# Kernel optimization log

Measured on AMD Instinct MI355X. Metric: run time of the kernel, lower is better.

## Reference

```python
import jax, jax.numpy as jnp
import numpy as np

B, D, NH, HD, L, P, FF = 2, 256, 8, 32, 4, 4, 1024
SPATIAL = np.array([[100, 100], [50, 50], [25, 25], [13, 13]], dtype=np.int64)
S_TOTAL = int(SPATIAL.prod(1).sum())  # 13294
EPS = 1e-5


def setup_inputs() -> dict:
    key = jax.random.key(0)
    ks = jax.random.split(key, 20)
    std = 0.02
    f32 = jnp.float32
    return {
        "query": jax.random.normal(ks[0], (B, S_TOTAL, D), f32),
        "query_pos": jax.random.normal(ks[1], (B, S_TOTAL, D), f32),
        "valid_ratios": jnp.ones((B, L, 2), f32),
        "spatial_shapes": SPATIAL,
        "level_start_index": np.concatenate([[0], SPATIAL.prod(1).cumsum()[:-1]]).astype(np.int64),
        "W_off": jax.random.normal(ks[2], (D, NH * L * P * 2), f32) * std,
        "b_off": jax.random.normal(ks[3], (NH * L * P * 2,), f32) * std,
        "W_attn": jax.random.normal(ks[4], (D, NH * L * P), f32) * std,
        "b_attn": jax.random.normal(ks[5], (NH * L * P,), f32) * std,
        "W_val": jax.random.normal(ks[6], (D, D), f32) * std,
        "b_val": jnp.zeros((D,), f32),
        "W_out": jax.random.normal(ks[7], (D, D), f32) * std,
        "b_out": jnp.zeros((D,), f32),
        "ln1_g": jnp.ones((D,), f32),
        "ln1_b": jnp.zeros((D,), f32),
        "W1": jax.random.normal(ks[8], (D, FF), f32) * std,
        "b1": jnp.zeros((FF,), f32),
        "W2": jax.random.normal(ks[9], (FF, D), f32) * std,
        "b2": jnp.zeros((D,), f32),
        "ln2_g": jnp.ones((D,), f32),
        "ln2_b": jnp.zeros((D,), f32),
    }


def _layer_norm(x, g, b):
    m = x.mean(-1, keepdims=True)
    v = ((x - m) ** 2).mean(-1, keepdims=True)
    return (x - m) * jax.lax.rsqrt(v + EPS) * g + b


def _bilinear_sample(v, loc, H, W):
    # v: [B, NH, H*W, HD]; loc: [B, NH, S, P, 2] normalized to [0,1]
    # Matches F.grid_sample(bilinear, padding_mode='zeros', align_corners=False)
    x = loc[..., 0] * W - 0.5
    y = loc[..., 1] * H - 0.5
    x0 = jnp.floor(x)
    y0 = jnp.floor(y)
    lx, ly = x - x0, y - y0
    x0i = x0.astype(jnp.int32)
    y0i = y0.astype(jnp.int32)
    x1i, y1i = x0i + 1, y0i + 1

    def corner(yi, xi, w):
        valid = (xi >= 0) & (xi < W) & (yi >= 0) & (yi < H)
        idx = jnp.clip(yi, 0, H - 1) * W + jnp.clip(xi, 0, W - 1)  # [B,NH,S,P]
        b_, h_, s_, p_ = idx.shape
        g = jnp.take_along_axis(v, idx.reshape(b_, h_, s_ * p_)[..., None], axis=2)
        g = g.reshape(b_, h_, s_, p_, -1)
        return g * (w * valid)[..., None]

    return (corner(y0i, x0i, (1 - lx) * (1 - ly)) + corner(y0i, x1i, lx * (1 - ly))
            + corner(y1i, x0i, (1 - lx) * ly) + corner(y1i, x1i, lx * ly))


def _forward(query, query_pos, valid_ratios, spatial_shapes,
             W_off, b_off, W_attn, b_attn, W_val, b_val, W_out, b_out,
             ln1_g, ln1_b, W1, b1, W2, b2, ln2_g, ln2_b):
    ss = np.asarray(spatial_shapes)
    Bq, S, _ = query.shape

    # ----- reference points (per-pixel centers, normalized by valid ratios) -----
    refs = []
    for lvl in range(ss.shape[0]):
        H, W = int(ss[lvl, 0]), int(ss[lvl, 1])
        ry, rx = jnp.meshgrid(jnp.linspace(0.5, H - 0.5, H), jnp.linspace(0.5, W - 0.5, W), indexing='ij')
        vy = valid_ratios[:, lvl, 1][:, None, None]
        vx = valid_ratios[:, lvl, 0][:, None, None]
        ry = ry[None] / (vy * H)
        rx = rx[None] / (vx * W)
        refs.append(jnp.stack((rx, ry), -1).reshape(Bq, H * W, 2))
    ref = jnp.concatenate(refs, 1)  # [B, S, 2] (identical across levels)

    # ----- multi-scale deformable attention -----
    q = query + query_pos
    v = (query @ W_val + b_val).reshape(Bq, S, NH, HD).transpose(0, 2, 1, 3)  # [B,NH,S,HD]
    off = (q @ W_off + b_off).reshape(Bq, S, NH, L, P, 2)
    aw = jax.nn.softmax((q @ W_attn + b_attn).reshape(Bq, S, NH, L * P), -1)
    aw = aw.reshape(Bq, S, NH, L, P)
    normalizer = jnp.asarray(ss[:, ::-1].copy(), jnp.float32)  # (W, H) per level
    loc = ref[:, :, None, None, None, :] + off / normalizer[None, None, None, :, None, :]  # [B,S,NH,L,P,2]

    starts = np.concatenate([[0], ss.prod(1).cumsum()[:-1]])
    out = jnp.zeros((Bq, NH, S, HD), query.dtype)
    for lvl in range(ss.shape[0]):
        H, W = int(ss[lvl, 0]), int(ss[lvl, 1])
        s0 = int(starts[lvl])
        v_l = v[:, :, s0:s0 + H * W]                       # [B,NH,HW,HD]
        loc_l = loc[:, :, :, lvl].transpose(0, 2, 1, 3, 4)  # [B,NH,S,P,2]
        samp = _bilinear_sample(v_l, loc_l, H, W)           # [B,NH,S,P,HD]
        w_l = aw[:, :, :, lvl].transpose(0, 2, 1, 3)        # [B,NH,S,P]
        out = out + (samp * w_l[..., None]).sum(3)
    attn_out = out.transpose(0, 2, 1, 3).reshape(Bq, S, D) @ W_out + b_out

    # ----- residual + LN + FFN + residual + LN -----
    x = _layer_norm(query + attn_out, ln1_g, ln1_b)
    f = jax.nn.relu(x @ W1 + b1) @ W2 + b2
    return _layer_norm(x + f, ln2_g, ln2_b)


def reference(query, query_pos, valid_ratios, spatial_shapes, level_start_index,
              W_off, b_off, W_attn, b_attn, W_val, b_val, W_out, b_out,
              ln1_g, ln1_b, W1, b1, W2, b2, ln2_g, ln2_b):
    return _forward(query, query_pos, valid_ratios, spatial_shapes,
                    W_off, b_off, W_attn, b_attn, W_val, b_val, W_out, b_out,
                    ln1_g, ln1_b, W1, b1, W2, b2, ln2_g, ln2_b)
```

## Files before the change

### kernel.cpp

```cpp
#include <hip/hip_runtime.h>
#include <math.h>

#define R_ROWS 26588
#define S_TOT  13294
#define NHEAD  8
#define NLVL   4
#define EPSF   1e-5f

typedef __attribute__((ext_vector_type(8))) short short8;
typedef __attribute__((ext_vector_type(4))) float f32x4;
typedef __attribute__((ext_vector_type(2))) float f32x2;
typedef unsigned short ushort_t;

__device__ __forceinline__ unsigned short f2bf(float f) {
    unsigned int u = __builtin_bit_cast(unsigned int, f);
    unsigned int r = (u + 0x7FFFu + ((u >> 16) & 1u)) >> 16;
    return (unsigned short)r;
}

__global__ __launch_bounds__(256) void prep_kernel(
    const float* __restrict__ W_val, const float* __restrict__ W_off,
    const float* __restrict__ W_attn, const float* __restrict__ W_out,
    const float* __restrict__ W1, const float* __restrict__ W2,
    ushort_t* __restrict__ wt_val, ushort_t* __restrict__ wt_off,
    ushort_t* __restrict__ wt_attn, ushort_t* __restrict__ wt_out,
    ushort_t* __restrict__ wt_w1, ushort_t* __restrict__ wt_w2,
    const float* __restrict__ query, const float* __restrict__ qpos,
    ushort_t* __restrict__ qry_bf, ushort_t* __restrict__ qsum_bf)
{
    __shared__ ushort_t tt[32][33];
    int bid = blockIdx.x;
    if (bid < 736) {
        const float* src; ushort_t* dst; int K, N, t;
        if (bid < 64)       { src = W_val;  dst = wt_val;  K = 256;  N = 256;  t = bid; }
        else if (bid < 128) { src = W_off;  dst = wt_off;  K = 256;  N = 256;  t = bid - 64; }
        else if (bid < 160) { src = W_attn; dst = wt_attn; K = 256;  N = 128;  t = bid - 128; }
        else if (bid < 224) { src = W_out;  dst = wt_out;  K = 256;  N = 256;  t = bid - 160; }
        else if (bid < 480) { src = W1;     dst = wt_w1;   K = 256;  N = 1024; t = bid - 224; }
        else                { src = W2;     dst = wt_w2;   K = 1024; N = 256;  t = bid - 480; }
        int nt = N / 32;
        int bn = (t % nt) * 32, bk = (t / nt) * 32;
        int x = threadIdx.x & 31;
        int y = threadIdx.x >> 5;
#pragma unroll
        for (int i = 0; i < 4; ++i) {
            int k = y + i * 8;
            tt[x][k] = f2bf(src[(long)(bk + k) * N + bn + x]);
        }
        __syncthreads();
#pragma unroll
        for (int i = 0; i < 4; ++i) {
            int n = y + i * 8;
            dst[(long)(bn + n) * K + bk + x] = tt[n][x];
        }
    } else {
        int i = (bid - 736) * 256 + threadIdx.x;
        float4 a = ((const float4*)query)[i];
        float4 b = ((const float4*)qpos)[i];
        uint2 qa, qs;
        qa.x = (unsigned)f2bf(a.x) | ((unsigned)f2bf(a.y) << 16);
        qa.y = (unsigned)f2bf(a.z) | ((unsigned)f2bf(a.w) << 16);
        qs.x = (unsigned)f2bf(a.x + b.x) | ((unsigned)f2bf(a.y + b.y) << 16);
        qs.y = (unsigned)f2bf(a.z + b.z) | ((unsigned)f2bf(a.w + b.w) << 16);
        ((uint2*)qry_bf)[i] = qa;
        ((uint2*)qsum_bf)[i] = qs;
    }
}

__device__ __forceinline__ void stage_ab(
    const ushort_t* __restrict__ Arow, const ushort_t* __restrict__ Brow,
    int K, int k0, ushort_t* As, ushort_t* Bs, int wave, int lane)
{
    int quadS = lane & 3;
    int rr = lane >> 2;
#pragma unroll
    for (int inst = 0; inst < 2; ++inst) {
        int base_row = wave * 32 + inst * 16;
        int r = base_row + rr;
        int quadG = quadS ^ ((r >> 1) & 3);
        const ushort_t* gp = Arow + (long)r * K + k0 + quadG * 8;
        __builtin_amdgcn_global_load_lds(
            (const __attribute__((address_space(1))) unsigned int*)gp,
            (__attribute__((address_space(3))) unsigned int*)&As[base_row * 32],
            16, 0, 0);
    }
#pragma unroll
    for (int inst = 0; inst < 2; ++inst) {
        int base_row = wave * 32 + inst * 16;
        int r = base_row + rr;
        int quadG = quadS ^ ((r >> 1) & 3);
        const ushort_t* gp = Brow + (long)r * K + k0 + quadG * 8;
        __builtin_amdgcn_global_load_lds(
            (const __attribute__((address_space(1))) unsigned int*)gp,
            (__attribute__((address_space(3))) unsigned int*)&Bs[base_row * 32],
            16, 0, 0);
    }
}

__device__ __forceinline__ void gemm_body(
    ushort_t* As, ushort_t* Bs,
    const ushort_t* __restrict__ A, const ushort_t* __restrict__ Wt,
    const float* __restrict__ bias, void* __restrict__ Cv,
    int M, int N, int K, int bm, int bn, bool out_bf16, bool relu)
{
    const int tid  = threadIdx.x;
    const int wave = tid >> 6;
    const int lane = tid & 63;
    const int l15  = lane & 15;
    const int quad = lane >> 4;
    const int wm   = (wave >> 1) * 64;
    const int wn   = (wave & 1) * 64;

    const ushort_t* Arow = A + (long)bm * K;
    const ushort_t* Brow = Wt + (long)bn * K;

    f32x4 acc[4][4];
#pragma unroll
    for (int i = 0; i < 4; ++i)
#pragma unroll
        for (int j = 0; j < 4; ++j) acc[i][j] = (f32x4)0.0f;

    int aoff[4], boff[4];
#pragma unroll
    for (int mi = 0; mi < 4; ++mi) {
        int r = wm + mi * 16 + l15;
        aoff[mi] = r * 32 + (quad ^ ((r >> 1) & 3)) * 8;
    }
#pragma unroll
    for (int ni = 0; ni < 4; ++ni) {
        int r = wn + ni * 16 + l15;
        boff[ni] = r * 32 + (quad ^ ((r >> 1) & 3)) * 8;
    }

    const int NT = K >> 5;
    stage_ab(Arow, Brow, K, 0,  As,        Bs,        wave, lane);
    stage_ab(Arow, Brow, K, 32, As + 4096, Bs + 4096, wave, lane);
    int cur = 0;
    for (int t = 0; t < NT; ++t) {
        if (t + 2 < NT) {
            int nb = cur + 2; if (nb >= 3) nb -= 3;
            stage_ab(Arow, Brow, K, (t + 2) << 5,
                     As + nb * 4096, Bs + nb * 4096, wave, lane);
            asm volatile("s_waitcnt vmcnt(8)" ::: "memory");
        } else if (t + 2 == NT) {
            asm volatile("s_waitcnt vmcnt(4)" ::: "memory");
        } else {
            asm volatile("s_waitcnt vmcnt(0)" ::: "memory");
        }
        asm volatile("s_barrier" ::: "memory");

        const ushort_t* Ab = As + cur * 4096;
        const ushort_t* Bb = Bs + cur * 4096;
        short8 af[4], bf[4];
#pragma unroll
        for (int mi = 0; mi < 4; ++mi) af[mi] = *(const short8*)&Ab[aoff[mi]];
#pragma unroll
        for (int ni = 0; ni < 4; ++ni) bf[ni] = *(const short8*)&Bb[boff[ni]];
#pragma unroll
        for (int mi = 0; mi < 4; ++mi)
#pragma unroll
            for (int ni = 0; ni < 4; ++ni)
                acc[mi][ni] = __builtin_amdgcn_mfma_f32_16x16x32_bf16(
                    af[mi], bf[ni], acc[mi][ni], 0, 0, 0);
        if (t + 3 < NT)
            asm volatile("s_barrier" ::: "memory");
        cur = cur + 1; if (cur >= 3) cur -= 3;
    }

#pragma unroll
    for (int mi = 0; mi < 4; ++mi) {
#pragma unroll
        for (int r = 0; r < 4; ++r) {
            int row = bm + wm + mi * 16 + quad * 4 + r;
            if (row >= M) continue;
#pragma unroll
            for (int ni = 0; ni < 4; ++ni) {
                int col = bn + wn + ni * 16 + l15;
                float vv = acc[mi][ni][r] + bias[col];
                if (relu) vv = fmaxf(vv, 0.f);
                if (out_bf16)
                    ((ushort_t*)Cv)[(long)row * N + col] = f2bf(vv);
                else
                    ((float*)Cv)[(long)row * N + col] = vv;
            }
        }
    }
}

template<bool OUT_BF16, bool RELU>
__global__ __launch_bounds__(256, 3) void gemm_mfma_kernel(
    const ushort_t* __restrict__ A, const ushort_t* __restrict__ Wt,
    const float* __restrict__ bias, void* __restrict__ Cv,
    int M, int N, int K)
{
    __shared__ ushort_t As[3 * 4096];
    __shared__ ushort_t Bs[3 * 4096];
    gemm_body(As, Bs, A, Wt, bias, Cv, M, N, K,
              blockIdx.x * 128, blockIdx.y * 128, OUT_BF16, RELU);
}

__global__ __launch_bounds__(256, 3) void proj_kernel(
    const ushort_t* __restrict__ qry_bf, const ushort_t* __restrict__ q_bf,
    const ushort_t* __restrict__ wt_val, const ushort_t* __restrict__ wt_off,
    const ushort_t* __restrict__ wt_attn,
    const float* __restrict__ b_val, const float* __restrict__ b_off,
    const float* __restrict__ b_attn,
    ushort_t* __restrict__ v_bf, float* __restrict__ cb, float* __restrict__ logits)
{
    __shared__ ushort_t As[3 * 4096];
    __shared__ ushort_t Bs[3 * 4096];
    int y = blockIdx.y;
    const ushort_t* A; const ushort_t* Wt; const float* bias;
    void* C; bool outbf; int N, bn;
    if (y < 2)      { A = qry_bf; Wt = wt_val;  bias = b_val;  C = v_bf;   outbf = true;  N = 256; bn = y * 128; }
    else if (y < 4) { A = q_bf;   Wt = wt_off;  bias = b_off;  C = cb;     outbf = false; N = 256; bn = (y - 2) * 128; }
    else            { A = q_bf;   Wt = wt_attn; bias = b_attn; C = logits; outbf = false; N = 128; bn = 0; }
    gemm_body(As, Bs, A, Wt, bias, C, R_ROWS, N, 256, blockIdx.x * 128, bn, outbf, false);
}

__device__ __forceinline__ void stage_ln64(
    const ushort_t* __restrict__ Arow, const ushort_t* __restrict__ Brow,
    int K, int k0, ushort_t* As, ushort_t* Bs, int wave, int lane)
{
    int quadS = lane & 3;
    int rr = lane >> 2;
    {
        int base_row = wave * 16;
        int r = base_row + rr;
        int quadG = quadS ^ ((r >> 1) & 3);
        const ushort_t* gp = Arow + (long)r * K + k0 + quadG * 8;
        __builtin_amdgcn_global_load_lds(
            (const __attribute__((address_space(1))) unsigned int*)gp,
            (__attribute__((address_space(3))) unsigned int*)&As[base_row * 32],
            16, 0, 0);
    }
#pragma unroll
    for (int inst = 0; inst < 4; ++inst) {
        int base_row = wave * 64 + inst * 16;
        int r = base_row + rr;
        int quadG = quadS ^ ((r >> 1) & 3);
        const ushort_t* gp = Brow + (long)r * K + k0 + quadG * 8;
        __builtin_amdgcn_global_load_lds(
            (const __attribute__((address_space(1))) unsigned int*)gp,
            (__attribute__((address_space(3))) unsigned int*)&Bs[base_row * 32],
            16, 0, 0);
    }
}

template<bool DUAL>
__global__ __launch_bounds__(256, 2) void gemm_ln_kernel(
    const ushort_t* __restrict__ A, const ushort_t* __restrict__ Wt,
    const float* __restrict__ bias, const float* __restrict__ resid,
    const float* __restrict__ gam, const float* __restrict__ bet,
    float* __restrict__ outf, ushort_t* __restrict__ outb,
    int M, int K)
{
    __shared__ ushort_t As[4 * 2048];
    __shared__ ushort_t Bs[3 * 8192];
    __shared__ float s1s[64][4], s2s[64][4];

    const int tid  = threadIdx.x;
    const int wave = tid >> 6;
    const int lane = tid & 63;
    const int l15  = lane & 15;
    const int quad = lane >> 4;
    const int wn   = wave * 64;
    const int bm   = blockIdx.x * 64;

    const ushort_t* Arow = A + (long)bm * K;

    float bias4[4], g4[4], be4[4];
#pragma unroll
    for (int ni = 0; ni < 4; ++ni) {
        int col = wn + ni * 16 + l15;
        bias4[ni] = bias[col];
        g4[ni]    = gam[col];
        be4[ni]   = bet[col];
    }
    float rv[4][4][4];
#pragma unroll
    for (int mi = 0; mi < 4; ++mi)
#pragma unroll
        for (int rr = 0; rr < 4; ++rr) {
            int row = bm + mi * 16 + quad * 4 + rr;
#pragma unroll
            for (int ni = 0; ni < 4; ++ni) {
                int col = wn + ni * 16 + l15;
                rv[mi][rr][ni] = (row < M) ? resid[(long)row * 256 + col] : 0.f;
            }
        }

    f32x4 acc[4][4];
#pragma unroll
    for (int i = 0; i < 4; ++i)
#pragma unroll
        for (int j = 0; j < 4; ++j) acc[i][j] = (f32x4)0.0f;

    int aoff[4], boff[4];
#pragma unroll
    for (int mi = 0; mi < 4; ++mi) {
        int r = mi * 16 + l15;
        aoff[mi] = r * 32 + (quad ^ ((r >> 1) & 3)) * 8;
    }
#pragma unroll
    for (int ni = 0; ni < 4; ++ni) {
        int r = wn + ni * 16 + l15;
        boff[ni] = r * 32 + (quad ^ ((r >> 1) & 3)) * 8;
    }

    const int NT = K >> 5;
    stage_ln64(Arow, Wt, K, 0,  As,        Bs,        wave, lane);
    stage_ln64(Arow, Wt, K, 32, As + 2048, Bs + 8192, wave, lane);
    int bcur = 0;
    for (int t = 0; t < NT; ++t) {
        const int acur = t & 3;
        if (t + 2 < NT) {
            int bnb = bcur + 2; if (bnb >= 3) bnb -= 3;
            stage_ln64(Arow, Wt, K, (t + 2) << 5,
                       As + ((t + 2) & 3) * 2048, Bs + bnb * 8192, wave, lane);
            asm volatile("s_waitcnt vmcnt(10)" ::: "memory");
        } else if (t + 2 == NT) {
            asm volatile("s_waitcnt vmcnt(5)" ::: "memory");
        } else {
            asm volatile("s_waitcnt vmcnt(0)" ::: "memory");
        }
        asm volatile("s_barrier" ::: "memory");

        const ushort_t* Ab = As + acur * 2048;
        const ushort_t* Bb = Bs + bcur * 8192;
        short8 af[4], bf[4];
#pragma unroll
        for (int mi = 0; mi < 4; ++mi) af[mi] = *(const short8*)&Ab[aoff[mi]];
#pragma unroll
        for (int ni = 0; ni < 4; ++ni) bf[ni] = *(const short8*)&Bb[boff[ni]];
#pragma unroll
        for (int mi = 0; mi < 4; ++mi)
#pragma unroll
            for (int ni = 0; ni < 4; ++ni)
                acc[mi][ni] = __builtin_amdgcn_mfma_f32_16x16x32_bf16(
                    af[mi], bf[ni], acc[mi][ni], 0, 0, 0);
        bcur = bcur + 1; if (bcur >= 3) bcur -= 3;
    }

#pragma unroll
    for (int mi = 0; mi < 4; ++mi)
#pragma unroll
        for (int rr = 0; rr < 4; ++rr) {
            float s1 = 0.f, s2 = 0.f;
#pragma unroll
            for (int ni = 0; ni < 4; ++ni) {
                float x = acc[mi][ni][rr] + bias4[ni] + rv[mi][rr][ni];
                acc[mi][ni][rr] = x;
                s1 += x; s2 += x * x;
            }
#pragma unroll
            for (int o = 1; o < 16; o <<= 1) {
                s1 += __shfl_xor(s1, o);
                s2 += __shfl_xor(s2, o);
            }
            if (l15 == 0) {
                int rl = mi * 16 + quad * 4 + rr;
                s1s[rl][wave] = s1;
                s2s[rl][wave] = s2;
            }
        }
    __syncthreads();
#pragma unroll
    for (int mi = 0; mi < 4; ++mi)
#pragma unroll
        for (int rr = 0; rr < 4; ++rr) {
            int rl  = mi * 16 + quad * 4 + rr;
            int row = bm + rl;
            float t1 = s1s[rl][0] + s1s[rl][1] + s1s[rl][2] + s1s[rl][3];
            float t2 = s2s[rl][0] + s2s[rl][1] + s2s[rl][2] + s2s[rl][3];
            float mean = t1 * (1.f / 256.f);
            float var  = t2 * (1.f / 256.f) - mean * mean;
            float inv  = rsqrtf(var + EPSF);
            if (row < M) {
#pragma unroll
                for (int ni = 0; ni < 4; ++ni) {
                    int col = wn + ni * 16 + l15;
                    float y = (acc[mi][ni][rr] - mean) * inv * g4[ni] + be4[ni];
                    outf[(long)row * 256 + col] = y;
                    if (DUAL) outb[(long)row * 256 + col] = f2bf(y);
                }
            }
        }
}

#define DEF_BLOCKS 6647

__global__ __launch_bounds__(256, 6) void deform_sample_kernel(
    const ushort_t* __restrict__ v, const float* __restrict__ off,
    const float* __restrict__ logits, const float* __restrict__ vr,
    ushort_t* __restrict__ out)
{
    const int Hs_[4] = {100, 50, 25, 13};
    const int S0_[4] = {0, 10000, 12500, 13125};

    __shared__ float meta[32 * 132];

    int bid = blockIdx.x;
    int wb  = (bid & 7) * 831 + (bid >> 3);
    int grp = wb * 32 + (threadIdx.x >> 3);
    int j    = threadIdx.x & 3;
    int half = (threadIdx.x >> 2) & 1;
    if (grp >= R_ROWS * NHEAD) return;
    int h = grp & 7;
    int r = grp >> 3;
    int b = (r >= S_TOT) ? 1 : 0;
    int s = r - b * S_TOT;

    int lq = (s < 10000) ? 0 : (s < 12500) ? 1 : (s < 13125) ? 2 : 3;
    int t  = s - S0_[lq];
    int Wq = Hs_[lq];
    int iy = t / Wq;
    int jx = t - iy * Wq;
    float vx = vr[(b * NLVL + lq) * 2 + 0];
    float vy = vr[(b * NLVL + lq) * 2 + 1];
    float rx = (jx + 0.5f) / (vx * (float)Wq);
    float ry = (iy + 0.5f) / (vy * (float)Wq);

    const float* offp = off + (long)r * 256 + h * 32;
    float4 op = ((const float4*)offp)[2 * j + half];
    float4 lg = ((const float4*)(logits + (long)grp * 16))[j];

    float mx = fmaxf(fmaxf(lg.x, lg.y), fmaxf(lg.z, lg.w));
    mx = fmaxf(mx, __shfl_xor(mx, 1));
    mx = fmaxf(mx, __shfl_xor(mx, 2));
    float l0 = half ? lg.z : lg.x;
    float l1 = half ? lg.w : lg.y;
    float e0 = __expf(l0 - mx), e1 = __expf(l1 - mx);
    float sl = e0 + e1;
    float s4 = sl + __shfl_xor(sl, 4);
    float sum = s4 + __shfl_xor(s4, 1);
    sum += __shfl_xor(sum, 2);
    float inv = 1.f / sum;

    const int   H  = Hs_[j];
    const float fH = (float)H;
    const int   s0 = S0_[j];
    const int   boff = b ? (S_TOT * 512) : 0;
    float oxs2[2] = {op.x, op.z};
    float oys2[2] = {op.y, op.w};
    float wts2[2] = {e0 * inv, e1 * inv};

    float* mg = &meta[(threadIdx.x >> 3) * 132];
#pragma unroll
    for (int ii = 0; ii < 2; ++ii) {
        float x = rx * fH + oxs2[ii] - 0.5f;
        float y = ry * fH + oys2[ii] - 0.5f;
        float xf = floorf(x), yf = floorf(y);
        float lx = x - xf, ly = y - yf;
        int x0 = (int)xf, y0 = (int)yf;
        bool xv0 = (x0 >= 0) & (x0 < H);
        bool xv1 = (x0 >= -1) & (x0 < H - 1);
        bool yv0 = (y0 >= 0) & (y0 < H);
        bool yv1 = (y0 >= -1) & (y0 < H - 1);
        float w = wts2[ii];
        f32x4 w4;
        w4.x = (xv0 & yv0) ? (1.f - lx) * (1.f - ly) * w : 0.f;
        w4.y = (xv1 & yv0) ? lx * (1.f - ly) * w : 0.f;
        w4.z = (xv0 & yv1) ? (1.f - lx) * ly * w : 0.f;
        w4.w = (xv1 & yv1) ? lx * ly * w : 0.f;
        int xc0 = min(max(x0, 0), H - 1), xc1 = min(max(x0 + 1, 0), H - 1);
        int yc0 = min(max(y0, 0), H - 1), yc1 = min(max(y0 + 1, 0), H - 1);
        int4 o4;
        o4.x = ((s0 + yc0 * H + xc0) << 9) + boff;
        o4.y = ((s0 + yc0 * H + xc1) << 9) + boff;
        o4.z = ((s0 + yc1 * H + xc0) << 9) + boff;
        o4.w = ((s0 + yc1 * H + xc1) << 9) + boff;
        int pt = 8 * half + 4 * ii + j;
        *(f32x4*)&mg[pt * 8]     = w4;
        *(int4*) &mg[pt * 8 + 4] = o4;
    }
    asm volatile("s_waitcnt lgkmcnt(0)" ::: "memory");

    const char* vbase = (const char*)v;
    const unsigned loff = (unsigned)(h * 64 + j * 16);
    f32x2 acc2[4];
#pragma unroll
    for (int c = 0; c < 4; ++c) acc2[c] = (f32x2)0.0f;

#define FMA4(G, WGT) do {                                                    \
        unsigned uu0 = (G).x, uu1 = (G).y, uu2 = (G).z, uu3 = (G).w;         \
        f32x2 gv;                                                            \
        gv.x = __builtin_bit_cast(float, uu0 << 16);                         \
        gv.y = __builtin_bit_cast(float, uu0 & 0xFFFF0000u);                 \
        acc2[0] += gv * (WGT);                                               \
        gv.x = __builtin_bit_cast(float, uu1 << 16);                         \
        gv.y = __builtin_bit_cast(float, uu1 & 0xFFFF0000u);                 \
        acc2[1] += gv * (WGT);                                               \
        gv.x = __builtin_bit_cast(float, uu2 << 16);                         \
        gv.y = __builtin_bit_cast(float, uu2 & 0xFFFF0000u);                 \
        acc2[2] += gv * (WGT);                                               \
        gv.x = __builtin_bit_cast(float, uu3 << 16);                         \
        gv.y = __builtin_bit_cast(float, uu3 & 0xFFFF0000u);                 \
        acc2[3] += gv * (WGT);                                               \
    } while (0)

    const float* ms = &mg[half * 64];
#pragma unroll
    for (int m = 0; m < 8; ++m) {
        f32x4 w4 = *(const f32x4*)&ms[m * 8];
        int4  o4 = *(const int4*) &ms[m * 8 + 4];
        uint4 g0 = *(const uint4*)(vbase + ((unsigned)o4.x + loff));
        uint4 g1 = *(const uint4*)(vbase + ((unsigned)o4.y + loff));
        uint4 g2 = *(const uint4*)(vbase + ((unsigned)o4.z + loff));
        uint4 g3 = *(const uint4*)(vbase + ((unsigned)o4.w + loff));
        FMA4(g0, w4.x); FMA4(g1, w4.y); FMA4(g2, w4.z); FMA4(g3, w4.w);
    }
#undef FMA4

#pragma unroll
    for (int c = 0; c < 4; ++c) {
        acc2[c].x += __shfl_xor(acc2[c].x, 4);
        acc2[c].y += __shfl_xor(acc2[c].y, 4);
    }
    if (half == 0) {
        uint4 o;
        o.x = (unsigned)f2bf(acc2[0].x) | ((unsigned)f2bf(acc2[0].y) << 16);
        o.y = (unsigned)f2bf(acc2[1].x) | ((unsigned)f2bf(acc2[1].y) << 16);
        o.z = (unsigned)f2bf(acc2[2].x) | ((unsigned)f2bf(acc2[2].y) << 16);
        o.w = (unsigned)f2bf(acc2[3].x) | ((unsigned)f2bf(acc2[3].y) << 16);
        *(uint4*)&out[(long)r * 256 + h * 32 + j * 8] = o;
    }
}

extern "C" void kernel_launch(void* const* d_in, const int* in_sizes, int n_in,
                              void* d_out, int out_size, void* d_ws, size_t ws_size,
                              hipStream_t stream)
{
    const float* query  = (const float*)d_in[0];
    const float* qpos   = (const float*)d_in[1];
    const float* vr     = (const float*)d_in[2];
    const float* W_off  = (const float*)d_in[5];
    const float* b_off  = (const float*)d_in[6];
    const float* W_attn = (const float*)d_in[7];
    const float* b_attn = (const float*)d_in[8];
    const float* W_val  = (const float*)d_in[9];
    const float* b_val  = (const float*)d_in[10];
    const float* W_out  = (const float*)d_in[11];
    const float* b_out  = (const float*)d_in[12];
    const float* ln1g   = (const float*)d_in[13];
    const float* ln1b   = (const float*)d_in[14];
    const float* W1     = (const float*)d_in[15];
    const float* b1     = (const float*)d_in[16];
    const float* W2     = (const float*)d_in[17];
    const float* b2     = (const float*)d_in[18];
    const float* ln2g   = (const float*)d_in[19];
    const float* ln2b   = (const float*)d_in[20];
    float* out = (float*)d_out;

    float* ws = (float*)d_ws;
    const long R128 = (long)R_ROWS * 128;
    ushort_t* q_bf    = (ushort_t*)(ws);
    ushort_t* qry_bf  = (ushort_t*)(ws + R128);
    ushort_t* v_bf    = (ushort_t*)(ws + 2 * R128);
    float*    logits  = ws + 3 * R128;
    ushort_t* h_bf    = (ushort_t*)(ws);
    float*    cb      = ws + 4 * R128;
    ushort_t* samp_bf = (ushort_t*)(ws + 6 * R128);
    float*    xb      = ws + 7 * R128;
    ushort_t* wt      = (ushort_t*)(ws + 9 * R128);
    ushort_t* wt_val  = wt;
    ushort_t* wt_off  = wt + 65536;
    ushort_t* wt_attn = wt + 131072;
    ushort_t* wt_out  = wt + 163840;
    ushort_t* wt_w1   = wt + 229376;
    ushort_t* wt_w2   = wt + 491520;

    dim3 blk(256);
    const int MB128 = (R_ROWS + 127) / 128;
    const int MB64  = (R_ROWS + 63) / 64;

    prep_kernel<<<736 + R_ROWS / 4, blk, 0, stream>>>(
        W_val, W_off, W_attn, W_out, W1, W2,
        wt_val, wt_off, wt_attn, wt_out, wt_w1, wt_w2,
        query, qpos, qry_bf, q_bf);
    proj_kernel<<<dim3(MB128, 5), blk, 0, stream>>>(
        qry_bf, q_bf, wt_val, wt_off, wt_attn, b_val, b_off, b_attn,
        v_bf, cb, logits);
    deform_sample_kernel<<<DEF_BLOCKS, blk, 0, stream>>>(
        v_bf, cb, logits, vr, samp_bf);
    gemm_ln_kernel<true><<<MB64, blk, 0, stream>>>(
        samp_bf, wt_out, b_out, query, ln1g, ln1b, xb, samp_bf, R_ROWS, 256);
    gemm_mfma_kernel<true, true><<<dim3(MB128, 8), blk, 0, stream>>>(
        samp_bf, wt_w1, b1, h_bf, R_ROWS, 1024, 256);
    gemm_ln_kernel<false><<<MB64, blk, 0, stream>>>(
        h_bf, wt_w2, b2, xb, ln2g, ln2b, out, nullptr, R_ROWS, 1024);
}
```

Baseline: 293.5 us.

## Split GEMM+LayerNorm kernel across eight waves with 32-column slices

The fused GEMM+LayerNorm kernel now launches 512 threads per block. Each of eight waves computes a 64x32 output slice instead of a 64x64 one, so the per-thread accumulator and residual register footprint is halved. The staging of A and B tiles and the vmcnt wait counts are redistributed to match, and the LayerNorm row reduction sums eight partials. The aim is more resident waves per CU to hide latency, at the cost of more shared-memory reloads of the A tile per wave and a larger cross-wave reduction.

```diff
diff --git a/kernel.cpp b/kernel.cpp
--- a/kernel.cpp
+++ b/kernel.cpp
@@ -218,13 +218,13 @@
     gemm_body(As, Bs, A, Wt, bias, C, R_ROWS, N, 256, blockIdx.x * 128, bn, outbf, false);
 }
 
-__device__ __forceinline__ void stage_ln64(
+__device__ __forceinline__ void stage_ln64_8w(
     const ushort_t* __restrict__ Arow, const ushort_t* __restrict__ Brow,
     int K, int k0, ushort_t* As, ushort_t* Bs, int wave, int lane)
 {
     int quadS = lane & 3;
     int rr = lane >> 2;
-    {
+    if (wave < 4) {
         int base_row = wave * 16;
         int r = base_row + rr;
         int quadG = quadS ^ ((r >> 1) & 3);
@@ -235,8 +235,8 @@
             16, 0, 0);
     }
 #pragma unroll
-    for (int inst = 0; inst < 4; ++inst) {
-        int base_row = wave * 64 + inst * 16;
+    for (int inst = 0; inst < 2; ++inst) {
+        int base_row = wave * 32 + inst * 16;
         int r = base_row + rr;
         int quadG = quadS ^ ((r >> 1) & 3);
         const ushort_t* gp = Brow + (long)r * K + k0 + quadG * 8;
@@ -248,7 +248,7 @@
 }
 
 template<bool DUAL>
-__global__ __launch_bounds__(256, 2) void gemm_ln_kernel(
+__global__ __launch_bounds__(512, 4) void gemm_ln_kernel(
     const ushort_t* __restrict__ A, const ushort_t* __restrict__ Wt,
     const float* __restrict__ bias, const float* __restrict__ resid,
     const float* __restrict__ gam, const float* __restrict__ bet,
@@ -257,70 +257,72 @@
 {
     __shared__ ushort_t As[4 * 2048];
     __shared__ ushort_t Bs[3 * 8192];
-    __shared__ float s1s[64][4], s2s[64][4];
+    __shared__ float s1s[64][8], s2s[64][8];
 
     const int tid  = threadIdx.x;
     const int wave = tid >> 6;
     const int lane = tid & 63;
     const int l15  = lane & 15;
     const int quad = lane >> 4;
-    const int wn   = wave * 64;
+    const int wn   = wave * 32;
     const int bm   = blockIdx.x * 64;
 
     const ushort_t* Arow = A + (long)bm * K;
 
-    float bias4[4], g4[4], be4[4];
-#pragma unroll
-    for (int ni = 0; ni < 4; ++ni) {
+    float bias2[2], g2[2], be2[2];
+#pragma unroll
+    for (int ni = 0; ni < 2; ++ni) {
         int col = wn + ni * 16 + l15;
-        bias4[ni] = bias[col];
-        g4[ni]    = gam[col];
-        be4[ni]   = bet[col];
-    }
-    float rv[4][4][4];
+        bias2[ni] = bias[col];
+        g2[ni]    = gam[col];
+        be2[ni]   = bet[col];
+    }
+    float rv[4][4][2];
 #pragma unroll
     for (int mi = 0; mi < 4; ++mi)
 #pragma unroll
         for (int rr = 0; rr < 4; ++rr) {
             int row = bm + mi * 16 + quad * 4 + rr;
 #pragma unroll
-            for (int ni = 0; ni < 4; ++ni) {
+            for (int ni = 0; ni < 2; ++ni) {
                 int col = wn + ni * 16 + l15;
                 rv[mi][rr][ni] = (row < M) ? resid[(long)row * 256 + col] : 0.f;
             }
         }
 
-    f32x4 acc[4][4];
+    f32x4 acc[4][2];
 #pragma unroll
     for (int i = 0; i < 4; ++i)
 #pragma unroll
-        for (int j = 0; j < 4; ++j) acc[i][j] = (f32x4)0.0f;
-
-    int aoff[4], boff[4];
+        for (int j = 0; j < 2; ++j) acc[i][j] = (f32x4)0.0f;
+
+    int aoff[4], boff[2];
 #pragma unroll
     for (int mi = 0; mi < 4; ++mi) {
         int r = mi * 16 + l15;
         aoff[mi] = r * 32 + (quad ^ ((r >> 1) & 3)) * 8;
     }
 #pragma unroll
-    for (int ni = 0; ni < 4; ++ni) {
+    for (int ni = 0; ni < 2; ++ni) {
         int r = wn + ni * 16 + l15;
         boff[ni] = r * 32 + (quad ^ ((r >> 1) & 3)) * 8;
     }
 
     const int NT = K >> 5;
-    stage_ln64(Arow, Wt, K, 0,  As,        Bs,        wave, lane);
-    stage_ln64(Arow, Wt, K, 32, As + 2048, Bs + 8192, wave, lane);
+    stage_ln64_8w(Arow, Wt, K, 0,  As,        Bs,        wave, lane);
+    stage_ln64_8w(Arow, Wt, K, 32, As + 2048, Bs + 8192, wave, lane);
     int bcur = 0;
     for (int t = 0; t < NT; ++t) {
         const int acur = t & 3;
         if (t + 2 < NT) {
             int bnb = bcur + 2; if (bnb >= 3) bnb -= 3;
-            stage_ln64(Arow, Wt, K, (t + 2) << 5,
-                       As + ((t + 2) & 3) * 2048, Bs + bnb * 8192, wave, lane);
-            asm volatile("s_waitcnt vmcnt(10)" ::: "memory");
+            stage_ln64_8w(Arow, Wt, K, (t + 2) << 5,
+                          As + ((t + 2) & 3) * 2048, Bs + bnb * 8192, wave, lane);
+            if (wave < 4) asm volatile("s_waitcnt vmcnt(6)" ::: "memory");
+            else          asm volatile("s_waitcnt vmcnt(4)" ::: "memory");
         } else if (t + 2 == NT) {
-            asm volatile("s_waitcnt vmcnt(5)" ::: "memory");
+            if (wave < 4) asm volatile("s_waitcnt vmcnt(3)" ::: "memory");
+            else          asm volatile("s_waitcnt vmcnt(2)" ::: "memory");
         } else {
             asm volatile("s_waitcnt vmcnt(0)" ::: "memory");
         }
@@ -328,15 +330,15 @@
 
         const ushort_t* Ab = As + acur * 2048;
         const ushort_t* Bb = Bs + bcur * 8192;
-        short8 af[4], bf[4];
+        short8 af[4], bf[2];
 #pragma unroll
         for (int mi = 0; mi < 4; ++mi) af[mi] = *(const short8*)&Ab[aoff[mi]];
 #pragma unroll
-        for (int ni = 0; ni < 4; ++ni) bf[ni] = *(const short8*)&Bb[boff[ni]];
+        for (int ni = 0; ni < 2; ++ni) bf[ni] = *(const short8*)&Bb[boff[ni]];
 #pragma unroll
         for (int mi = 0; mi < 4; ++mi)
 #pragma unroll
-            for (int ni = 0; ni < 4; ++ni)
+            for (int ni = 0; ni < 2; ++ni)
                 acc[mi][ni] = __builtin_amdgcn_mfma_f32_16x16x32_bf16(
                     af[mi], bf[ni], acc[mi][ni], 0, 0, 0);
         bcur = bcur + 1; if (bcur >= 3) bcur -= 3;
@@ -348,8 +350,8 @@
         for (int rr = 0; rr < 4; ++rr) {
             float s1 = 0.f, s2 = 0.f;
 #pragma unroll
-            for (int ni = 0; ni < 4; ++ni) {
-                float x = acc[mi][ni][rr] + bias4[ni] + rv[mi][rr][ni];
+            for (int ni = 0; ni < 2; ++ni) {
+                float x = acc[mi][ni][rr] + bias2[ni] + rv[mi][rr][ni];
                 acc[mi][ni][rr] = x;
                 s1 += x; s2 += x * x;
             }
@@ -371,16 +373,18 @@
         for (int rr = 0; rr < 4; ++rr) {
             int rl  = mi * 16 + quad * 4 + rr;
             int row = bm + rl;
-            float t1 = s1s[rl][0] + s1s[rl][1] + s1s[rl][2] + s1s[rl][3];
-            float t2 = s2s[rl][0] + s2s[rl][1] + s2s[rl][2] + s2s[rl][3];
+            float t1 = s1s[rl][0] + s1s[rl][1] + s1s[rl][2] + s1s[rl][3]
+                     + s1s[rl][4] + s1s[rl][5] + s1s[rl][6] + s1s[rl][7];
+            float t2 = s2s[rl][0] + s2s[rl][1] + s2s[rl][2] + s2s[rl][3]
+                     + s2s[rl][4] + s2s[rl][5] + s2s[rl][6] + s2s[rl][7];
             float mean = t1 * (1.f / 256.f);
             float var  = t2 * (1.f / 256.f) - mean * mean;
             float inv  = rsqrtf(var + EPSF);
             if (row < M) {
 #pragma unroll
-                for (int ni = 0; ni < 4; ++ni) {
+                for (int ni = 0; ni < 2; ++ni) {
                     int col = wn + ni * 16 + l15;
-                    float y = (acc[mi][ni][rr] - mean) * inv * g4[ni] + be4[ni];
+                    float y = (acc[mi][ni][rr] - mean) * inv * g2[ni] + be2[ni];
                     outf[(long)row * 256 + col] = y;
                     if (DUAL) outb[(long)row * 256 + col] = f2bf(y);
                 }
@@ -571,6 +575,7 @@
     ushort_t* wt_w2   = wt + 491520;
 
     dim3 blk(256);
+    dim3 blk512(512);
     const int MB128 = (R_ROWS + 127) / 128;
     const int MB64  = (R_ROWS + 63) / 64;
 
@@ -583,10 +588,10 @@
         v_bf, cb, logits);
     deform_sample_kernel<<<DEF_BLOCKS, blk, 0, stream>>>(
         v_bf, cb, logits, vr, samp_bf);
-    gemm_ln_kernel<true><<<MB64, blk, 0, stream>>>(
+    gemm_ln_kernel<true><<<MB64, blk512, 0, stream>>>(
         samp_bf, wt_out, b_out, query, ln1g, ln1b, xb, samp_bf, R_ROWS, 256);
     gemm_mfma_kernel<true, true><<<dim3(MB128, 8), blk, 0, stream>>>(
         samp_bf, wt_w1, b1, h_bf, R_ROWS, 1024, 256);
-    gemm_ln_kernel<false><<<MB64, blk, 0, stream>>>(
+    gemm_ln_kernel<false><<<MB64, blk512, 0, stream>>>(
         h_bf, wt_w2, b2, xb, ln2g, ln2b, out, nullptr, R_ROWS, 1024);
 }
```

New measurement: 298.3 us. Within noise of the previous version (+1.6%).
